# Optimization experiments

Measured on AMD Instinct MI355X. Metric: run time of the kernel, lower is better.

The kernel has to match this reference:

```python
import jax, jax.numpy as jnp
import numpy as np

N_LIG, N_TGT, E = 100000, 20000, 250000
LIG_IN, TGT_IN, H = 4, 1280, 128


def setup_inputs() -> dict:
    key = jax.random.key(0)
    ks = jax.random.split(key, 12)
    def lin_w(k, fan_in, fan_out):
        # kaiming-uniform-ish init, stored as [in, out] for x @ W
        bound = 1.0 / np.sqrt(fan_in)
        return jax.random.uniform(k, (fan_in, fan_out), jnp.float32, -bound, bound)
    return {
        "x_ligand": jax.random.normal(ks[0], (N_LIG, LIG_IN), jnp.float32),
        "x_target": jax.random.normal(ks[1], (N_TGT, TGT_IN), jnp.float32),
        "edge_src": jax.random.randint(ks[2], (E,), 0, N_LIG, jnp.int32),
        "edge_dst": jax.random.randint(ks[3], (E,), 0, N_TGT, jnp.int32),
        # SAGEConv (ligand -> target): lin_l on aggregated ligand msgs, lin_r on target self
        "W_lt_l": lin_w(ks[4], LIG_IN, H),
        "b_lt_l": jnp.zeros((H,), jnp.float32),
        "W_lt_r": lin_w(ks[5], TGT_IN, H),
        # SAGEConv (target -> ligand): lin_l on aggregated target msgs, lin_r on ligand self
        "W_tl_l": lin_w(ks[6], TGT_IN, H),
        "b_tl_l": jnp.zeros((H,), jnp.float32),
        "W_tl_r": lin_w(ks[7], LIG_IN, H),
        # edge predictor: Linear(2H -> 1)
        "W_ep": lin_w(ks[8], 2 * H, 1),
        "b_ep": jnp.zeros((1,), jnp.float32),
    }


def _mean_agg(x_src, src_idx, dst_idx, num_dst):
    # gather per-edge source features, scatter-mean onto destination nodes
    msg = x_src[src_idx]                                             # [E, F]
    s = jax.ops.segment_sum(msg, dst_idx, num_segments=num_dst)      # [N_dst, F]
    cnt = jax.ops.segment_sum(jnp.ones((src_idx.shape[0], 1), x_src.dtype),
                              dst_idx, num_segments=num_dst)         # [N_dst, 1]
    return s / jnp.maximum(cnt, 1.0)


def reference(x_ligand, x_target, edge_src, edge_dst,
              W_lt_l, b_lt_l, W_lt_r, W_tl_l, b_tl_l, W_tl_r, W_ep, b_ep):
    # SAGEConv (ligand, binds_to, target): aggregate ligand msgs into targets
    agg_t = _mean_agg(x_ligand, edge_src, edge_dst, N_TGT)           # [N_TGT, LIG_IN]
    t_out = agg_t @ W_lt_l + b_lt_l + x_target @ W_lt_r              # [N_TGT, H]
    # SAGEConv (target, binds_to, ligand): reversed edges (flip(0))
    agg_l = _mean_agg(x_target, edge_dst, edge_src, N_LIG)           # [N_LIG, TGT_IN]
    l_out = agg_l @ W_tl_l + b_tl_l + x_ligand @ W_tl_r              # [N_LIG, H]
    l_out = jax.nn.relu(l_out)
    t_out = jax.nn.relu(t_out)
    # edge predictor: gather endpoints, concat, linear, squeeze
    edge_feats = jnp.concatenate([l_out[edge_src], t_out[edge_dst]], axis=-1)  # [E, 2H]
    out = (edge_feats @ W_ep + b_ep).squeeze(-1)                     # [E]
    return out
```

## Files before the change

### kernel.cpp

```cpp
#include <hip/hip_runtime.h>
#include <hip/hip_bf16.h>


#define H 128
#define K_DIM 1280
#define LIG_IN 4
#define CAP_L 24
#define CAP_T 48
#define NCH 20

typedef __attribute__((ext_vector_type(8))) short bf16x8;
typedef __attribute__((ext_vector_type(4))) float f32x4;

#define AS1(p) ((const __attribute__((address_space(1))) void*)(p))
#define AS3(p) ((__attribute__((address_space(3))) void*)(p))

__global__ void fill_both(const int* __restrict__ src, const int* __restrict__ dst,
                          int* __restrict__ cur_l, int* __restrict__ cur_t,
                          int* __restrict__ adjd, int* __restrict__ adjs, int E)
{
    int e = blockIdx.x * blockDim.x + threadIdx.x;
    if (e >= E) return;
    int s = src[e], d = dst[e];
    int p = atomicAdd(&cur_l[s], 1);
    adjd[s * CAP_L + p] = d;
    int q = atomicAdd(&cur_t[d], 1);
    adjs[d * CAP_T + q] = s;
}

__global__ void cast_wt(const float* __restrict__ Wl, const float* __restrict__ Wr,
                        __hip_bfloat16* __restrict__ Wt, int n)
{
    int idx = blockIdx.x * blockDim.x + threadIdx.x;
    if (idx >= n) return;
    int nr = idx / K_DIM, k = idx - nr * K_DIM;
    float v = (nr < H) ? Wl[k * H + nr] : Wr[k * H + (nr - H)];
    Wt[idx] = __float2bfloat16(v);
}

__device__ inline bf16x8 cvt8(float4 u, float4 v)
{
    union { __hip_bfloat16 h[8]; bf16x8 f; } r;
    r.h[0] = __float2bfloat16(u.x); r.h[1] = __float2bfloat16(u.y);
    r.h[2] = __float2bfloat16(u.z); r.h[3] = __float2bfloat16(u.w);
    r.h[4] = __float2bfloat16(v.x); r.h[5] = __float2bfloat16(v.y);
    r.h[6] = __float2bfloat16(v.z); r.h[7] = __float2bfloat16(v.w);
    return r.f;
}

__global__ __launch_bounds__(256)
void gemm_fused(const float* __restrict__ Xf,
                const unsigned short* __restrict__ Wt,
                float* __restrict__ y_tl, float* __restrict__ t_lin, int M)
{
    __shared__ float As[32 * 64];
    __shared__ short Bs[128 * 64];

    const int t = threadIdx.x;
    const int w = t >> 6, lane = t & 63;
    const int m16 = lane & 15, q = lane >> 4;
    const int wn = w;
    const int mb = blockIdx.x >> 1, nb = blockIdx.x & 1;
    const int bm = mb * 32;
    const int nb128 = nb * 128;

    const float* a_g[2];
#pragma unroll
    for (int i = 0; i < 2; ++i) {
        int slot = i * 256 + w * 64 + lane;
        int m = slot >> 4, cl = slot & 15;
        int cg = cl ^ (m & 15);
        int row = min(bm + m, M - 1);
        a_g[i] = Xf + (size_t)row * K_DIM + cg * 4;
    }
    const unsigned short* b_g[4];
#pragma unroll
    for (int i = 0; i < 4; ++i) {
        int slot = i * 256 + w * 64 + lane;
        int n = slot >> 3, cl = slot & 7;
        int cg = cl ^ (n & 7);
        b_g[i] = Wt + (size_t)(nb128 + n) * K_DIM + cg * 8;
    }

    f32x4 acc[2][2];
#pragma unroll
    for (int i = 0; i < 2; ++i)
#pragma unroll
        for (int j = 0; j < 2; ++j)
            acc[i][j] = (f32x4){0.f, 0.f, 0.f, 0.f};

#pragma unroll
    for (int i = 0; i < 2; ++i)
        __builtin_amdgcn_global_load_lds(AS1(a_g[i]), AS3((char*)As + (i * 256 + w * 64) * 16), 16, 0, 0);
#pragma unroll
    for (int i = 0; i < 4; ++i)
        __builtin_amdgcn_global_load_lds(AS1(b_g[i]), AS3((char*)Bs + (i * 256 + w * 64) * 16), 16, 0, 0);
    __syncthreads();

    for (int ch = 0; ch < NCH; ++ch) {
#pragma unroll
        for (int ks = 0; ks < 2; ++ks) {
            bf16x8 aF[2];
#pragma unroll
            for (int i = 0; i < 2; ++i) {
                int row = i * 16 + m16;
                int c = ks * 8 + q * 2;
                int s0 = row * 16 + (c ^ m16);
                int s1 = s0 ^ 1;
                float4 u = *(const float4*)((const char*)As + s0 * 16);
                float4 v = *(const float4*)((const char*)As + s1 * 16);
                aF[i] = cvt8(u, v);
            }
            bf16x8 bF[2];
#pragma unroll
            for (int j = 0; j < 2; ++j) {
                int n = wn * 32 + j * 16 + m16;
                int c = ks * 4 + q;
                int s = n * 8 + (c ^ (n & 7));
                bF[j] = *(const bf16x8*)((const char*)Bs + s * 16);
            }
#pragma unroll
            for (int i = 0; i < 2; ++i)
#pragma unroll
                for (int j = 0; j < 2; ++j)
                    acc[i][j] = __builtin_amdgcn_mfma_f32_16x16x32_bf16(aF[i], bF[j], acc[i][j], 0, 0, 0);
        }
        __syncthreads();
        if (ch + 1 < NCH) {
            const int kc = (ch + 1) * 64;
#pragma unroll
            for (int i = 0; i < 2; ++i)
                __builtin_amdgcn_global_load_lds(AS1(a_g[i] + kc),
                                                 AS3((char*)As + (i * 256 + w * 64) * 16), 16, 0, 0);
#pragma unroll
            for (int i = 0; i < 4; ++i)
                __builtin_amdgcn_global_load_lds(AS1(b_g[i] + kc),
                                                 AS3((char*)Bs + (i * 256 + w * 64) * 16), 16, 0, 0);
            __syncthreads();
        }
    }

    float* __restrict__ Y = nb ? t_lin : y_tl;
#pragma unroll
    for (int i = 0; i < 2; ++i) {
#pragma unroll
        for (int j = 0; j < 2; ++j) {
            int col = wn * 32 + j * 16 + m16;
#pragma unroll
            for (int r = 0; r < 4; ++r) {
                int row = bm + i * 16 + q * 4 + r;
                if (row < M) Y[(size_t)row * H + col] = acc[i][j][r];
            }
        }
    }
}

__global__ void target_post(const int* __restrict__ cur_t, const int* __restrict__ adjs,
                            const float* __restrict__ xl, const float* __restrict__ t_lin,
                            const float* __restrict__ W_lt_l, const float* __restrict__ b_lt_l,
                            const float* __restrict__ W_ep,
                            float* __restrict__ st, int NT)
{
    int wid = (blockIdx.x * blockDim.x + threadIdx.x) >> 6;
    int lane = threadIdx.x & 63;
    if (wid >= NT) return;
    int cnt = cur_t[wid];
    float a0 = 0.f, a1 = 0.f, a2 = 0.f, a3 = 0.f;
    for (int j = lane; j < cnt; j += 64) {
        int s = adjs[wid * CAP_T + j];
        float4 v = *(const float4*)(xl + (size_t)s * LIG_IN);
        a0 += v.x; a1 += v.y; a2 += v.z; a3 += v.w;
    }
#pragma unroll
    for (int off = 32; off > 0; off >>= 1) {
        a0 += __shfl_xor(a0, off);
        a1 += __shfl_xor(a1, off);
        a2 += __shfl_xor(a2, off);
        a3 += __shfl_xor(a3, off);
    }
    float inv = 1.0f / fmaxf((float)cnt, 1.0f);
    a0 *= inv; a1 *= inv; a2 *= inv; a3 *= inv;
    float acc = 0.f;
#pragma unroll
    for (int p = 0; p < 2; ++p) {
        int h = lane + p * 64;
        float v = a0 * W_lt_l[h] + a1 * W_lt_l[H + h] + a2 * W_lt_l[2 * H + h] +
                  a3 * W_lt_l[3 * H + h] + b_lt_l[h] + t_lin[(size_t)wid * H + h];
        v = fmaxf(v, 0.f);
        acc += v * W_ep[H + h];
    }
#pragma unroll
    for (int off = 32; off > 0; off >>= 1) acc += __shfl_down(acc, off);
    if (lane == 0) st[wid] = acc;
}

__global__ void ligand_gather_post(const int* __restrict__ cur_l, const int* __restrict__ adjd,
                                   const float* __restrict__ y_tl,
                                   const float* __restrict__ xl,
                                   const float* __restrict__ W_tl_r, const float* __restrict__ b_tl_l,
                                   const float* __restrict__ W_ep,
                                   float* __restrict__ sl, int NL)
{
    int wid = (blockIdx.x * blockDim.x + threadIdx.x) >> 6;
    int lane = threadIdx.x & 63;
    if (wid >= NL) return;
    int cnt = cur_l[wid];
    float a0 = 0.f, a1 = 0.f;
    for (int j = 0; j < cnt; ++j) {
        int d = adjd[wid * CAP_L + j];
        float2 f = ((const float2*)(y_tl + (size_t)d * H))[lane];
        a0 += f.x;
        a1 += f.y;
    }
    float inv = 1.0f / fmaxf((float)cnt, 1.0f);
    float4 x = *(const float4*)(xl + (size_t)wid * LIG_IN);
    float acc = 0.f;
    {
        int h = 2 * lane;
        float v = a0 * inv + b_tl_l[h] +
                  x.x * W_tl_r[h] + x.y * W_tl_r[H + h] +
                  x.z * W_tl_r[2 * H + h] + x.w * W_tl_r[3 * H + h];
        v = fmaxf(v, 0.f);
        acc += v * W_ep[h];
    }
    {
        int h = 2 * lane + 1;
        float v = a1 * inv + b_tl_l[h] +
                  x.x * W_tl_r[h] + x.y * W_tl_r[H + h] +
                  x.z * W_tl_r[2 * H + h] + x.w * W_tl_r[3 * H + h];
        v = fmaxf(v, 0.f);
        acc += v * W_ep[h];
    }
#pragma unroll
    for (int off = 32; off > 0; off >>= 1) acc += __shfl_down(acc, off);
    if (lane == 0) sl[wid] = acc;
}

__global__ void edge_out(const int* __restrict__ src, const int* __restrict__ dst,
                         const float* __restrict__ sl, const float* __restrict__ st,
                         const float* __restrict__ b_ep, float* __restrict__ out, int E)
{
    int e = blockIdx.x * blockDim.x + threadIdx.x;
    if (e >= E) return;
    out[e] = sl[src[e]] + st[dst[e]] + b_ep[0];
}

extern "C" void kernel_launch(void* const* d_in, const int* in_sizes, int n_in,
                              void* d_out, int out_size, void* d_ws, size_t ws_size,
                              hipStream_t stream) {
    const float* x_ligand = (const float*)d_in[0];
    const float* x_target = (const float*)d_in[1];
    const int*   edge_src = (const int*)d_in[2];
    const int*   edge_dst = (const int*)d_in[3];
    const float* W_lt_l   = (const float*)d_in[4];
    const float* b_lt_l   = (const float*)d_in[5];
    const float* W_lt_r   = (const float*)d_in[6];
    const float* W_tl_l   = (const float*)d_in[7];
    const float* b_tl_l   = (const float*)d_in[8];
    const float* W_tl_r   = (const float*)d_in[9];
    const float* W_ep     = (const float*)d_in[10];
    const float* b_ep     = (const float*)d_in[11];
    float* out = (float*)d_out;

    const int NL = in_sizes[0] / LIG_IN;
    const int NT = in_sizes[1] / K_DIM;
    const int E  = in_sizes[2];

    char* ws = (char*)d_ws;
    size_t off = 0;
    auto take = [&](size_t bytes) { size_t o = off; off += (bytes + 15) & ~(size_t)15; return o; };
    size_t off_Wt     = take((size_t)2 * H * K_DIM * 2);
    size_t off_y_tl   = take((size_t)NT * H * 4);
    size_t off_t_lin  = take((size_t)NT * H * 4);
    size_t off_adjd   = take((size_t)NL * CAP_L * 4);
    size_t off_adjs   = take((size_t)NT * CAP_T * 4);
    size_t off_cur_l  = take((size_t)NL * 4);
    size_t off_cur_t  = take((size_t)NT * 4);
    size_t off_sl     = take((size_t)NL * 4);
    size_t off_st     = take((size_t)NT * 4);
    if (off > ws_size) {
        hipMemsetAsync(d_out, 0, (size_t)out_size * 4, stream);
        return;
    }

    __hip_bfloat16* Wt = (__hip_bfloat16*)(ws + off_Wt);
    float* y_tl  = (float*)(ws + off_y_tl);
    float* t_lin = (float*)(ws + off_t_lin);
    int*   adjd  = (int*)(ws + off_adjd);
    int*   adjs  = (int*)(ws + off_adjs);
    int*   cur_l = (int*)(ws + off_cur_l);
    int*   cur_t = (int*)(ws + off_cur_t);
    float* sl    = (float*)(ws + off_sl);
    float* st    = (float*)(ws + off_st);

    hipMemsetAsync(cur_l, 0, off_sl - off_cur_l, stream);

    int nw = 2 * H * K_DIM;
    cast_wt<<<(nw + 255) / 256, 256, 0, stream>>>(W_tl_l, W_lt_r, Wt, nw);

    gemm_fused<<<((NT + 31) / 32) * 2, 256, 0, stream>>>(x_target, (const unsigned short*)Wt,
                                                         y_tl, t_lin, NT);

    fill_both<<<(E + 255) / 256, 256, 0, stream>>>(edge_src, edge_dst,
                                                   cur_l, cur_t, adjd, adjs, E);

    target_post<<<(NT * 64 + 255) / 256, 256, 0, stream>>>(cur_t, adjs, x_ligand, t_lin,
                                                           W_lt_l, b_lt_l, W_ep, st, NT);
    ligand_gather_post<<<(NL * 64 + 255) / 256, 256, 0, stream>>>(cur_l, adjd, y_tl, x_ligand,
                                                                  W_tl_r, b_tl_l, W_ep, sl, NL);
    edge_out<<<(E + 255) / 256, 256, 0, stream>>>(edge_src, edge_dst, sl, st, b_ep, out, E);
}
```

Baseline: 308.2 us.

## Merge prep and post kernels, replace LDS-staged GEMM with direct global loads

```diff
diff --git a/kernel.cpp b/kernel.cpp
--- a/kernel.cpp
+++ b/kernel.cpp
@@ -7,35 +7,32 @@
 #define LIG_IN 4
 #define CAP_L 24
 #define CAP_T 48
-#define NCH 20
 
 typedef __attribute__((ext_vector_type(8))) short bf16x8;
 typedef __attribute__((ext_vector_type(4))) float f32x4;
 
-#define AS1(p) ((const __attribute__((address_space(1))) void*)(p))
-#define AS3(p) ((__attribute__((address_space(3))) void*)(p))
-
-__global__ void fill_both(const int* __restrict__ src, const int* __restrict__ dst,
-                          int* __restrict__ cur_l, int* __restrict__ cur_t,
-                          int* __restrict__ adjd, int* __restrict__ adjs, int E)
-{
-    int e = blockIdx.x * blockDim.x + threadIdx.x;
-    if (e >= E) return;
-    int s = src[e], d = dst[e];
-    int p = atomicAdd(&cur_l[s], 1);
-    adjd[s * CAP_L + p] = d;
-    int q = atomicAdd(&cur_t[d], 1);
-    adjs[d * CAP_T + q] = s;
-}
-
-__global__ void cast_wt(const float* __restrict__ Wl, const float* __restrict__ Wr,
-                        __hip_bfloat16* __restrict__ Wt, int n)
-{
-    int idx = blockIdx.x * blockDim.x + threadIdx.x;
-    if (idx >= n) return;
-    int nr = idx / K_DIM, k = idx - nr * K_DIM;
-    float v = (nr < H) ? Wl[k * H + nr] : Wr[k * H + (nr - H)];
-    Wt[idx] = __float2bfloat16(v);
+__global__ void prep(const int* __restrict__ src, const int* __restrict__ dst,
+                     int* __restrict__ cur_l, int* __restrict__ cur_t,
+                     int* __restrict__ adjd, int* __restrict__ adjs, int E, int nb_fill,
+                     const float* __restrict__ Wl, const float* __restrict__ Wr,
+                     __hip_bfloat16* __restrict__ Wt, int nw)
+{
+    int b = blockIdx.x;
+    if (b < nb_fill) {
+        int e = b * blockDim.x + threadIdx.x;
+        if (e >= E) return;
+        int s = src[e], d = dst[e];
+        int p = atomicAdd(&cur_l[s], 1);
+        adjd[s * CAP_L + p] = d;
+        int q = atomicAdd(&cur_t[d], 1);
+        adjs[d * CAP_T + q] = s;
+    } else {
+        int idx = (b - nb_fill) * blockDim.x + threadIdx.x;
+        if (idx >= nw) return;
+        int nr = idx / K_DIM, k = idx - nr * K_DIM;
+        float v = (nr < H) ? Wl[k * H + nr] : Wr[k * H + (nr - H)];
+        Wt[idx] = __float2bfloat16(v);
+    }
 }
 
 __device__ inline bf16x8 cvt8(float4 u, float4 v)
@@ -49,38 +46,23 @@
 }
 
 __global__ __launch_bounds__(256)
-void gemm_fused(const float* __restrict__ Xf,
-                const unsigned short* __restrict__ Wt,
-                float* __restrict__ y_tl, float* __restrict__ t_lin, int M)
-{
-    __shared__ float As[32 * 64];
-    __shared__ short Bs[128 * 64];
-
+void gemm_direct(const float* __restrict__ Xf,
+                 const unsigned short* __restrict__ Wt,
+                 float* __restrict__ y_tl, float* __restrict__ t_lin, int M)
+{
     const int t = threadIdx.x;
     const int w = t >> 6, lane = t & 63;
     const int m16 = lane & 15, q = lane >> 4;
-    const int wn = w;
     const int mb = blockIdx.x >> 1, nb = blockIdx.x & 1;
     const int bm = mb * 32;
-    const int nb128 = nb * 128;
-
-    const float* a_g[2];
-#pragma unroll
-    for (int i = 0; i < 2; ++i) {
-        int slot = i * 256 + w * 64 + lane;
-        int m = slot >> 4, cl = slot & 15;
-        int cg = cl ^ (m & 15);
-        int row = min(bm + m, M - 1);
-        a_g[i] = Xf + (size_t)row * K_DIM + cg * 4;
-    }
-    const unsigned short* b_g[4];
-#pragma unroll
-    for (int i = 0; i < 4; ++i) {
-        int slot = i * 256 + w * 64 + lane;
-        int n = slot >> 3, cl = slot & 7;
-        int cg = cl ^ (n & 7);
-        b_g[i] = Wt + (size_t)(nb128 + n) * K_DIM + cg * 8;
-    }
+    const int col0 = nb * 128 + w * 32;
+
+    const int r0 = min(bm + m16,      M - 1);
+    const int r1 = min(bm + m16 + 16, M - 1);
+    const float* a0 = Xf + (size_t)r0 * K_DIM + q * 8;
+    const float* a1 = Xf + (size_t)r1 * K_DIM + q * 8;
+    const unsigned short* b0 = Wt + (size_t)(col0 + m16)      * K_DIM + q * 8;
+    const unsigned short* b1 = Wt + (size_t)(col0 + m16 + 16) * K_DIM + q * 8;
 
     f32x4 acc[2][2];
 #pragma unroll
@@ -89,55 +71,21 @@
         for (int j = 0; j < 2; ++j)
             acc[i][j] = (f32x4){0.f, 0.f, 0.f, 0.f};
 
-#pragma unroll
-    for (int i = 0; i < 2; ++i)
-        __builtin_amdgcn_global_load_lds(AS1(a_g[i]), AS3((char*)As + (i * 256 + w * 64) * 16), 16, 0, 0);
-#pragma unroll
-    for (int i = 0; i < 4; ++i)
-        __builtin_amdgcn_global_load_lds(AS1(b_g[i]), AS3((char*)Bs + (i * 256 + w * 64) * 16), 16, 0, 0);
-    __syncthreads();
-
-    for (int ch = 0; ch < NCH; ++ch) {
-#pragma unroll
-        for (int ks = 0; ks < 2; ++ks) {
-            bf16x8 aF[2];
-#pragma unroll
-            for (int i = 0; i < 2; ++i) {
-                int row = i * 16 + m16;
-                int c = ks * 8 + q * 2;
-                int s0 = row * 16 + (c ^ m16);
-                int s1 = s0 ^ 1;
-                float4 u = *(const float4*)((const char*)As + s0 * 16);
-                float4 v = *(const float4*)((const char*)As + s1 * 16);
-                aF[i] = cvt8(u, v);
-            }
-            bf16x8 bF[2];
-#pragma unroll
-            for (int j = 0; j < 2; ++j) {
-                int n = wn * 32 + j * 16 + m16;
-                int c = ks * 4 + q;
-                int s = n * 8 + (c ^ (n & 7));
-                bF[j] = *(const bf16x8*)((const char*)Bs + s * 16);
-            }
-#pragma unroll
-            for (int i = 0; i < 2; ++i)
-#pragma unroll
-                for (int j = 0; j < 2; ++j)
-                    acc[i][j] = __builtin_amdgcn_mfma_f32_16x16x32_bf16(aF[i], bF[j], acc[i][j], 0, 0, 0);
-        }
-        __syncthreads();
-        if (ch + 1 < NCH) {
-            const int kc = (ch + 1) * 64;
-#pragma unroll
-            for (int i = 0; i < 2; ++i)
-                __builtin_amdgcn_global_load_lds(AS1(a_g[i] + kc),
-                                                 AS3((char*)As + (i * 256 + w * 64) * 16), 16, 0, 0);
-#pragma unroll
-            for (int i = 0; i < 4; ++i)
-                __builtin_amdgcn_global_load_lds(AS1(b_g[i] + kc),
-                                                 AS3((char*)Bs + (i * 256 + w * 64) * 16), 16, 0, 0);
-            __syncthreads();
-        }
+#pragma unroll 2
+    for (int ks = 0; ks < K_DIM / 32; ++ks) {
+        const int k = ks * 32;
+        float4 u0 = *(const float4*)(a0 + k);
+        float4 v0 = *(const float4*)(a0 + k + 4);
+        float4 u1 = *(const float4*)(a1 + k);
+        float4 v1 = *(const float4*)(a1 + k + 4);
+        bf16x8 B0 = *(const bf16x8*)(b0 + k);
+        bf16x8 B1 = *(const bf16x8*)(b1 + k);
+        bf16x8 A0 = cvt8(u0, v0);
+        bf16x8 A1 = cvt8(u1, v1);
+        acc[0][0] = __builtin_amdgcn_mfma_f32_16x16x32_bf16(A0, B0, acc[0][0], 0, 0, 0);
+        acc[0][1] = __builtin_amdgcn_mfma_f32_16x16x32_bf16(A0, B1, acc[0][1], 0, 0, 0);
+        acc[1][0] = __builtin_amdgcn_mfma_f32_16x16x32_bf16(A1, B0, acc[1][0], 0, 0, 0);
+        acc[1][1] = __builtin_amdgcn_mfma_f32_16x16x32_bf16(A1, B1, acc[1][1], 0, 0, 0);
     }
 
     float* __restrict__ Y = nb ? t_lin : y_tl;
@@ -145,7 +93,7 @@
     for (int i = 0; i < 2; ++i) {
 #pragma unroll
         for (int j = 0; j < 2; ++j) {
-            int col = wn * 32 + j * 16 + m16;
+            int col = w * 32 + j * 16 + m16;
 #pragma unroll
             for (int r = 0; r < 4; ++r) {
                 int row = bm + i * 16 + q * 4 + r;
@@ -155,85 +103,82 @@
     }
 }
 
-__global__ void target_post(const int* __restrict__ cur_t, const int* __restrict__ adjs,
-                            const float* __restrict__ xl, const float* __restrict__ t_lin,
-                            const float* __restrict__ W_lt_l, const float* __restrict__ b_lt_l,
-                            const float* __restrict__ W_ep,
-                            float* __restrict__ st, int NT)
-{
-    int wid = (blockIdx.x * blockDim.x + threadIdx.x) >> 6;
+__global__ void post_both(const int* __restrict__ cur_t, const int* __restrict__ adjs,
+                          const int* __restrict__ cur_l, const int* __restrict__ adjd,
+                          const float* __restrict__ xl,
+                          const float* __restrict__ t_lin, const float* __restrict__ y_tl,
+                          const float* __restrict__ W_lt_l, const float* __restrict__ b_lt_l,
+                          const float* __restrict__ W_tl_r, const float* __restrict__ b_tl_l,
+                          const float* __restrict__ W_ep,
+                          float* __restrict__ st, float* __restrict__ sl,
+                          int NT, int NL, int nb_t)
+{
     int lane = threadIdx.x & 63;
-    if (wid >= NT) return;
-    int cnt = cur_t[wid];
-    float a0 = 0.f, a1 = 0.f, a2 = 0.f, a3 = 0.f;
-    for (int j = lane; j < cnt; j += 64) {
-        int s = adjs[wid * CAP_T + j];
-        float4 v = *(const float4*)(xl + (size_t)s * LIG_IN);
-        a0 += v.x; a1 += v.y; a2 += v.z; a3 += v.w;
-    }
-#pragma unroll
-    for (int off = 32; off > 0; off >>= 1) {
-        a0 += __shfl_xor(a0, off);
-        a1 += __shfl_xor(a1, off);
-        a2 += __shfl_xor(a2, off);
-        a3 += __shfl_xor(a3, off);
-    }
-    float inv = 1.0f / fmaxf((float)cnt, 1.0f);
-    a0 *= inv; a1 *= inv; a2 *= inv; a3 *= inv;
-    float acc = 0.f;
-#pragma unroll
-    for (int p = 0; p < 2; ++p) {
-        int h = lane + p * 64;
-        float v = a0 * W_lt_l[h] + a1 * W_lt_l[H + h] + a2 * W_lt_l[2 * H + h] +
-                  a3 * W_lt_l[3 * H + h] + b_lt_l[h] + t_lin[(size_t)wid * H + h];
-        v = fmaxf(v, 0.f);
-        acc += v * W_ep[H + h];
-    }
-#pragma unroll
-    for (int off = 32; off > 0; off >>= 1) acc += __shfl_down(acc, off);
-    if (lane == 0) st[wid] = acc;
-}
-
-__global__ void ligand_gather_post(const int* __restrict__ cur_l, const int* __restrict__ adjd,
-                                   const float* __restrict__ y_tl,
-                                   const float* __restrict__ xl,
-                                   const float* __restrict__ W_tl_r, const float* __restrict__ b_tl_l,
-                                   const float* __restrict__ W_ep,
-                                   float* __restrict__ sl, int NL)
-{
-    int wid = (blockIdx.x * blockDim.x + threadIdx.x) >> 6;
-    int lane = threadIdx.x & 63;
-    if (wid >= NL) return;
-    int cnt = cur_l[wid];
-    float a0 = 0.f, a1 = 0.f;
-    for (int j = 0; j < cnt; ++j) {
-        int d = adjd[wid * CAP_L + j];
-        float2 f = ((const float2*)(y_tl + (size_t)d * H))[lane];
-        a0 += f.x;
-        a1 += f.y;
-    }
-    float inv = 1.0f / fmaxf((float)cnt, 1.0f);
-    float4 x = *(const float4*)(xl + (size_t)wid * LIG_IN);
-    float acc = 0.f;
-    {
-        int h = 2 * lane;
-        float v = a0 * inv + b_tl_l[h] +
-                  x.x * W_tl_r[h] + x.y * W_tl_r[H + h] +
-                  x.z * W_tl_r[2 * H + h] + x.w * W_tl_r[3 * H + h];
-        v = fmaxf(v, 0.f);
-        acc += v * W_ep[h];
-    }
-    {
-        int h = 2 * lane + 1;
-        float v = a1 * inv + b_tl_l[h] +
-                  x.x * W_tl_r[h] + x.y * W_tl_r[H + h] +
-                  x.z * W_tl_r[2 * H + h] + x.w * W_tl_r[3 * H + h];
-        v = fmaxf(v, 0.f);
-        acc += v * W_ep[h];
-    }
-#pragma unroll
-    for (int off = 32; off > 0; off >>= 1) acc += __shfl_down(acc, off);
-    if (lane == 0) sl[wid] = acc;
+    if ((int)blockIdx.x < nb_t) {
+        int wid = (blockIdx.x * blockDim.x + threadIdx.x) >> 6;
+        if (wid >= NT) return;
+        int cnt = cur_t[wid];
+        float a0 = 0.f, a1 = 0.f, a2 = 0.f, a3 = 0.f;
+        for (int j = lane; j < cnt; j += 64) {
+            int s = adjs[wid * CAP_T + j];
+            float4 v = *(const float4*)(xl + (size_t)s * LIG_IN);
+            a0 += v.x; a1 += v.y; a2 += v.z; a3 += v.w;
+        }
+#pragma unroll
+        for (int off = 32; off > 0; off >>= 1) {
+            a0 += __shfl_xor(a0, off);
+            a1 += __shfl_xor(a1, off);
+            a2 += __shfl_xor(a2, off);
+            a3 += __shfl_xor(a3, off);
+        }
+        float inv = 1.0f / fmaxf((float)cnt, 1.0f);
+        a0 *= inv; a1 *= inv; a2 *= inv; a3 *= inv;
+        float acc = 0.f;
+#pragma unroll
+        for (int p = 0; p < 2; ++p) {
+            int h = lane + p * 64;
+            float v = a0 * W_lt_l[h] + a1 * W_lt_l[H + h] + a2 * W_lt_l[2 * H + h] +
+                      a3 * W_lt_l[3 * H + h] + b_lt_l[h] + t_lin[(size_t)wid * H + h];
+            v = fmaxf(v, 0.f);
+            acc += v * W_ep[H + h];
+        }
+#pragma unroll
+        for (int off = 32; off > 0; off >>= 1) acc += __shfl_down(acc, off);
+        if (lane == 0) st[wid] = acc;
+    } else {
+        int wid = (((int)blockIdx.x - nb_t) * blockDim.x + threadIdx.x) >> 6;
+        if (wid >= NL) return;
+        int cnt = cur_l[wid];
+        float a0 = 0.f, a1 = 0.f;
+        for (int j = 0; j < cnt; ++j) {
+            int d = adjd[wid * CAP_L + j];
+            float2 f = ((const float2*)(y_tl + (size_t)d * H))[lane];
+            a0 += f.x;
+            a1 += f.y;
+        }
+        float inv = 1.0f / fmaxf((float)cnt, 1.0f);
+        float4 x = *(const float4*)(xl + (size_t)wid * LIG_IN);
+        float acc = 0.f;
+        {
+            int h = 2 * lane;
+            float v = a0 * inv + b_tl_l[h] +
+                      x.x * W_tl_r[h] + x.y * W_tl_r[H + h] +
+                      x.z * W_tl_r[2 * H + h] + x.w * W_tl_r[3 * H + h];
+            v = fmaxf(v, 0.f);
+            acc += v * W_ep[h];
+        }
+        {
+            int h = 2 * lane + 1;
+            float v = a1 * inv + b_tl_l[h] +
+                      x.x * W_tl_r[h] + x.y * W_tl_r[H + h] +
+                      x.z * W_tl_r[2 * H + h] + x.w * W_tl_r[3 * H + h];
+            v = fmaxf(v, 0.f);
+            acc += v * W_ep[h];
+        }
+#pragma unroll
+        for (int off = 32; off > 0; off >>= 1) acc += __shfl_down(acc, off);
+        if (lane == 0) sl[wid] = acc;
+    }
 }
 
 __global__ void edge_out(const int* __restrict__ src, const int* __restrict__ dst,
@@ -296,17 +241,21 @@
     hipMemsetAsync(cur_l, 0, off_sl - off_cur_l, stream);
 
     int nw = 2 * H * K_DIM;
-    cast_wt<<<(nw + 255) / 256, 256, 0, stream>>>(W_tl_l, W_lt_r, Wt, nw);
-
-    gemm_fused<<<((NT + 31) / 32) * 2, 256, 0, stream>>>(x_target, (const unsigned short*)Wt,
-                                                         y_tl, t_lin, NT);
-
-    fill_both<<<(E + 255) / 256, 256, 0, stream>>>(edge_src, edge_dst,
-                                                   cur_l, cur_t, adjd, adjs, E);
-
-    target_post<<<(NT * 64 + 255) / 256, 256, 0, stream>>>(cur_t, adjs, x_ligand, t_lin,
-                                                           W_lt_l, b_lt_l, W_ep, st, NT);
-    ligand_gather_post<<<(NL * 64 + 255) / 256, 256, 0, stream>>>(cur_l, adjd, y_tl, x_ligand,
-                                                                  W_tl_r, b_tl_l, W_ep, sl, NL);
+    int nb_fill = (E + 255) / 256;
+    int nb_cast = (nw + 255) / 256;
+    prep<<<nb_fill + nb_cast, 256, 0, stream>>>(edge_src, edge_dst, cur_l, cur_t,
+                                                adjd, adjs, E, nb_fill,
+                                                W_tl_l, W_lt_r, Wt, nw);
+
+    gemm_direct<<<((NT + 31) / 32) * 2, 256, 0, stream>>>(x_target, (const unsigned short*)Wt,
+                                                          y_tl, t_lin, NT);
+
+    int nb_t = (NT * 64 + 255) / 256;
+    int nb_l = (NL * 64 + 255) / 256;
+    post_both<<<nb_t + nb_l, 256, 0, stream>>>(cur_t, adjs, cur_l, adjd, x_ligand,
+                                               t_lin, y_tl, W_lt_l, b_lt_l,
+                                               W_tl_r, b_tl_l, W_ep, st, sl,
+                                               NT, NL, nb_t);
+
     edge_out<<<(E + 255) / 256, 256, 0, stream>>>(edge_src, edge_dst, sl, st, b_ep, out, E);
 }
```

Measured after the change: 376.4 us. 1.22x slower.
